# Optimization experiments

Measured on AMD Instinct MI355X. Metric: run time of the kernel, lower is better.

## Reference

```python
import jax, jax.numpy as jnp
import numpy as np

C = 0.1          # curvature
EPS = 1e-8
BN_EPS = 1e-5
MAX_NORM = 0.9

def batchnorm_train(x, gamma, beta):
    mu = jnp.mean(x, axis=0)
    var = jnp.var(x, axis=0)  # biased, matches torch BN normalization
    return gamma * (x - mu) * jax.lax.rsqrt(var + BN_EPS) + beta

def euclidean_to_poincare(x, c=C, max_norm=MAX_NORM):
    norm = jnp.linalg.norm(x, axis=-1, keepdims=True)
    zeros_mask = norm == 0
    safe_norm = jnp.where(zeros_mask, jnp.ones_like(norm), norm)
    sqrt_c = jnp.sqrt(jnp.asarray(c, x.dtype))
    scale = max_norm * jnp.tanh(sqrt_c * norm) / (sqrt_c * safe_norm)
    return jnp.where(zeros_mask, jnp.zeros_like(x), scale * x)

def poincare_to_euclidean(x, c=C):
    norms = jnp.linalg.norm(x, axis=-1, keepdims=True)
    norms = jnp.clip(norms, 1e-8, 1.0 - 1e-8)
    sqrt_c = jnp.sqrt(jnp.asarray(c, x.dtype))
    return x * jnp.arctanh(sqrt_c * norms) / (sqrt_c * norms)

def batch_poincare_exp_map(x, v, c=C):
    x_nsq = jnp.sum(x * x, axis=-1, keepdims=True)
    lambda_x = 2.0 / (1.0 - c * x_nsq + EPS)
    v_norm = jnp.linalg.norm(v, axis=-1, keepdims=True)
    v_norm = jnp.maximum(v_norm, EPS)
    sqrt_c = jnp.sqrt(jnp.asarray(c, x.dtype))
    scale = jnp.tanh(sqrt_c * lambda_x * v_norm / 2.0) / (sqrt_c * v_norm)
    sv = scale * v
    numerator = (1.0 - c * x_nsq) * sv
    x_sv = jnp.sum(x * sv, axis=-1, keepdims=True)
    sv_nsq = jnp.sum(sv * sv, axis=-1, keepdims=True)
    denom = 1.0 - 2.0 * c * x_sv + c * c * x_nsq * sv_nsq
    result = x + numerator / (denom + EPS)
    mask = jnp.all(jnp.isfinite(result), axis=-1, keepdims=True)
    return jnp.where(mask, result, jnp.zeros_like(result))

def batch_poincare_log_map(x, y, c=C):
    x_nsq = jnp.sum(x * x, axis=-1, keepdims=True)
    lambda_x = 2.0 / (1.0 - c * x_nsq + EPS)
    y_nsq = jnp.sum(y * y, axis=-1, keepdims=True)
    xy = jnp.sum(x * y, axis=-1, keepdims=True)
    numerator = (1.0 - 2.0 * c * xy + c * y_nsq) * x - (1.0 - c * x_nsq) * y
    denom = 1.0 - 2.0 * c * xy + c * c * x_nsq * y_nsq
    diff = numerator / (denom + EPS)
    diff_norm = jnp.linalg.norm(diff, axis=-1, keepdims=True)
    diff_norm = jnp.maximum(diff_norm, EPS)
    sqrt_c = jnp.sqrt(jnp.asarray(c, x.dtype))
    return 2.0 / (sqrt_c * lambda_x) * jnp.arctanh(sqrt_c * diff_norm) * diff / diff_norm

def setup_inputs() -> dict:
    key = jax.random.key(0)
    ks = jax.random.split(key, 8)
    B, D_IN, H, D_OUT = 8192, 1024, 2048, 1000
    x = jax.random.normal(ks[0], (B, D_IN), dtype=jnp.float32)
    # kaiming_normal fan_out: std = sqrt(2/fan_out) with fan_out = out_features
    W1 = jax.random.normal(ks[1], (H, D_IN), dtype=jnp.float32) * np.sqrt(2.0 / H)
    b1 = jnp.zeros((H,), jnp.float32)
    g1 = jnp.ones((H,), jnp.float32)
    be1 = jnp.zeros((H,), jnp.float32)
    W2 = jax.random.normal(ks[2], (H, H), dtype=jnp.float32) * np.sqrt(2.0 / H)
    b2 = jnp.zeros((H,), jnp.float32)
    g2 = jnp.ones((H,), jnp.float32)
    be2 = jnp.zeros((H,), jnp.float32)
    W3 = jax.random.normal(ks[3], (D_OUT, H), dtype=jnp.float32) * np.sqrt(2.0 / D_OUT)
    b3 = jnp.zeros((D_OUT,), jnp.float32)
    return {"x": x, "W1": W1, "b1": b1, "g1": g1, "be1": be1,
            "W2": W2, "b2": b2, "g2": g2, "be2": be2, "W3": W3, "b3": b3}

def reference(x, W1, b1, g1, be1, W2, b2, g2, be2, W3, b3):
    h1 = jax.nn.relu(batchnorm_train(x @ W1.T + b1, g1, be1))
    h1_hyp = euclidean_to_poincare(h1)
    origin = jnp.zeros_like(h1_hyp)
    h1_tan = batch_poincare_log_map(origin, h1_hyp)
    h2_tan = jax.nn.relu(batchnorm_train(h1_tan @ W2.T + b2, g2, be2))
    h2_hyp = batch_poincare_exp_map(origin, h2_tan)
    h2_euc = poincare_to_euclidean(h2_hyp)
    out = h2_euc @ W3.T + b3
    return jax.nn.log_softmax(out, axis=1)
```

## Files before the change

kernel.cpp:

```cpp
#include <hip/hip_runtime.h>

typedef __bf16 bf16x8 __attribute__((ext_vector_type(8)));
typedef float f32x16 __attribute__((ext_vector_type(16)));
typedef unsigned short us8 __attribute__((ext_vector_type(8)));

#define AS1 __attribute__((address_space(1)))
#define AS3 __attribute__((address_space(3)))

__device__ __forceinline__ unsigned short f2bf(float x) {
  unsigned int u = __float_as_uint(x);
  u += 0x7fffu + ((u >> 16) & 1u);
  return (unsigned short)(u >> 16);
}
__device__ __forceinline__ float bf2f(unsigned short u) {
  return __uint_as_float(((unsigned int)u) << 16);
}
__device__ __forceinline__ void async_copy16(const void* g, void* l) {
  __builtin_amdgcn_global_load_lds((AS1 void*)(g), (AS3 void*)(l), 16, 0, 0);
}

__global__ void __launch_bounds__(256) k_prep(const float* __restrict__ x,
                                              const float* __restrict__ W1,
                                              const float* __restrict__ W2,
                                              const float* __restrict__ W3,
                                              unsigned short* __restrict__ Xb,
                                              unsigned short* __restrict__ W1b,
                                              unsigned short* __restrict__ W2b,
                                              unsigned short* __restrict__ W3b,
                                              float* __restrict__ P) {
  const long n1 = 2097152, n2 = 524288, n3 = 1048576, n4 = 524288;
  long i = (long)blockIdx.x * 256 + threadIdx.x;
  const float* s = nullptr;
  unsigned short* d = nullptr;
  long j = i;
  if (i < n1)                { s = x;  d = Xb; }
  else if ((j -= n1) < n2)   { s = W1; d = W1b; }
  else if ((j -= n2) < n3)   { s = W2; d = W2b; }
  else if ((j -= n3) < n4) {
    ushort4 o;
    if ((j >> 9) < 1000) {
      float4 v = ((const float4*)W3)[j];
      o.x = f2bf(v.x); o.y = f2bf(v.y); o.z = f2bf(v.z); o.w = f2bf(v.w);
    } else { o.x = 0; o.y = 0; o.z = 0; o.w = 0; }
    ((ushort4*)W3b)[j] = o;
    return;
  } else {
    j -= n4;
    ((float4*)P)[j] = (float4){0.f, 0.f, 0.f, 0.f};
    return;
  }
  float4 v = ((const float4*)s)[j];
  ushort4 o;
  o.x = f2bf(v.x); o.y = f2bf(v.y); o.z = f2bf(v.z); o.w = f2bf(v.w);
  ((ushort4*)d)[j] = o;
}

template <bool OUTBF16, bool STATS>
__global__ void __launch_bounds__(256) k_gemm(const unsigned short* __restrict__ A,
                                              const unsigned short* __restrict__ B,
                                              void* __restrict__ Cout, int K,
                                              int lda, int ldb, int ldc, int nmax,
                                              const float* __restrict__ bias,
                                              float* __restrict__ P) {
  __shared__ __align__(16) unsigned short lA[128 * 64];
  __shared__ __align__(16) unsigned short lB[128 * 64];
  const int tid = threadIdx.x;
  const int wave = tid >> 6;
  const int lane = tid & 63;
  const long m0 = (long)blockIdx.y * 128;
  const long n0 = (long)blockIdx.x * 128;

  const int rsub = lane >> 3;
  const int qg = ((lane & 7) ^ rsub) * 8;
  const unsigned short* gA = A + (m0 + wave * 32 + rsub) * (long)lda + qg;
  const unsigned short* gB = B + (n0 + wave * 32 + rsub) * (long)ldb + qg;
  unsigned short* lAw = lA + (wave * 32) * 64;
  unsigned short* lBw = lB + (wave * 32) * 64;

  const int wr = (wave >> 1) * 64;
  const int wc = (wave & 1) * 64;
  const int l31 = lane & 31;
  const int khalf = lane >> 5;
  const int r7 = l31 & 7;

  f32x16 acc[2][2];
#pragma unroll
  for (int i = 0; i < 2; ++i)
#pragma unroll
    for (int j = 0; j < 2; ++j) acc[i][j] = (f32x16)(0.f);

  for (int k0 = 0; k0 < K; k0 += 64) {
#pragma unroll
    for (int r = 0; r < 4; ++r) {
      async_copy16(gA + (long)(r * 8) * lda + k0, lAw + r * 8 * 64);
      async_copy16(gB + (long)(r * 8) * ldb + k0, lBw + r * 8 * 64);
    }
    __syncthreads();

#pragma unroll
    for (int ks = 0; ks < 4; ++ks) {
      const int off = ((ks * 2 + khalf) ^ r7) * 8;
      bf16x8 af[2], bfr[2];
#pragma unroll
      for (int i = 0; i < 2; ++i)
        af[i] = *(const bf16x8*)&lA[(wr + i * 32 + l31) * 64 + off];
#pragma unroll
      for (int j = 0; j < 2; ++j)
        bfr[j] = *(const bf16x8*)&lB[(wc + j * 32 + l31) * 64 + off];
#pragma unroll
      for (int i = 0; i < 2; ++i)
#pragma unroll
        for (int j = 0; j < 2; ++j)
          acc[i][j] = __builtin_amdgcn_mfma_f32_32x32x16_bf16(af[i], bfr[j], acc[i][j], 0, 0, 0);
    }
    __syncthreads();
  }

  const int rbase = 4 * khalf;
  if (OUTBF16) {
    unsigned short* C = (unsigned short*)Cout;
#pragma unroll
    for (int i = 0; i < 2; ++i)
#pragma unroll
      for (int j = 0; j < 2; ++j) {
        long col = n0 + wc + j * 32 + l31;
#pragma unroll
        for (int reg = 0; reg < 16; ++reg) {
          long row = m0 + wr + i * 32 + (reg & 3) + 8 * (reg >> 2) + rbase;
          C[row * (long)ldc + col] = f2bf(acc[i][j][reg]);
        }
      }
  } else {
    float* C = (float*)Cout;
#pragma unroll
    for (int i = 0; i < 2; ++i)
#pragma unroll
      for (int j = 0; j < 2; ++j) {
        long col = n0 + wc + j * 32 + l31;
        if (col < nmax) {
          float bv = bias ? bias[col] : 0.f;
#pragma unroll
          for (int reg = 0; reg < 16; ++reg) {
            long row = m0 + wr + i * 32 + (reg & 3) + 8 * (reg >> 2) + rbase;
            C[row * (long)ldc + col] = acc[i][j][reg] + bv;
          }
        }
      }
  }

  if (STATS) {
    float* sred = (float*)lA;
    sred[tid] = 0.f;
    __syncthreads();
#pragma unroll
    for (int j = 0; j < 2; ++j) {
      float s = 0.f, s2 = 0.f;
#pragma unroll
      for (int i = 0; i < 2; ++i)
#pragma unroll
        for (int reg = 0; reg < 16; ++reg) {
          float v = acc[i][j][reg];
          s += v;
          s2 = fmaf(v, v, s2);
        }
      int cl = wc + j * 32 + l31;
      atomicAdd(&sred[cl], s);
      atomicAdd(&sred[128 + cl], s2);
    }
    __syncthreads();
    if (tid < 128) {
      atomicAdd(&P[n0 + tid], sred[tid]);
      atomicAdd(&P[2048 + n0 + tid], sred[128 + tid]);
    }
  }
}

__global__ void __launch_bounds__(256) k_bnfin(const float* __restrict__ P,
                                               const float* __restrict__ g,
                                               const float* __restrict__ be,
                                               float* __restrict__ sc,
                                               float* __restrict__ sh) {
  int col = blockIdx.x * 256 + threadIdx.x;
  float mean = P[col] * (1.f / 8192.f);
  float var = P[2048 + col] * (1.f / 8192.f) - mean * mean;
  float rinv = rsqrtf(var + 1e-5f);
  float a = g[col] * rinv;
  sc[col] = a;
  sh[col] = be[col] - mean * a;
}

template <bool STAGE2>
__global__ void __launch_bounds__(256) k_fuse(const unsigned short* __restrict__ Zb,
                                              const float* __restrict__ sc,
                                              const float* __restrict__ sh,
                                              unsigned short* __restrict__ Ab) {
  __shared__ float red[4];
  int row = blockIdx.x, t = threadIdx.x;
  us8 z8 = ((const us8*)(Zb + (long)row * 2048))[t];
  float4 a0 = ((const float4*)sc)[2 * t], a1 = ((const float4*)sc)[2 * t + 1];
  float4 b0 = ((const float4*)sh)[2 * t], b1 = ((const float4*)sh)[2 * t + 1];
  float v[8];
  v[0] = fmaxf(fmaf(bf2f(z8[0]), a0.x, b0.x), 0.f);
  v[1] = fmaxf(fmaf(bf2f(z8[1]), a0.y, b0.y), 0.f);
  v[2] = fmaxf(fmaf(bf2f(z8[2]), a0.z, b0.z), 0.f);
  v[3] = fmaxf(fmaf(bf2f(z8[3]), a0.w, b0.w), 0.f);
  v[4] = fmaxf(fmaf(bf2f(z8[4]), a1.x, b1.x), 0.f);
  v[5] = fmaxf(fmaf(bf2f(z8[5]), a1.y, b1.y), 0.f);
  v[6] = fmaxf(fmaf(bf2f(z8[6]), a1.z, b1.z), 0.f);
  v[7] = fmaxf(fmaf(bf2f(z8[7]), a1.w, b1.w), 0.f);
  float ss = 0.f;
#pragma unroll
  for (int i = 0; i < 8; ++i) ss = fmaf(v[i], v[i], ss);
#pragma unroll
  for (int o = 32; o > 0; o >>= 1) ss += __shfl_down(ss, o, 64);
  if ((t & 63) == 0) red[t >> 6] = ss;
  __syncthreads();
  float n2 = red[0] + red[1] + red[2] + red[3];

  const float rsc = 0.31622776601683794f;
  float fac;
  if (STAGE2) {
    float nn = sqrtf(n2);
    float vn = fmaxf(nn, 1e-8f);
    float tt = rsc * vn;
    float scl = tanhf(tt) / tt;
    float hn = scl * nn;
    float cn = fminf(fmaxf(hn, 1e-8f), 1.0f);
    float z = rsc * cn;
    fac = scl * (atanhf(z) / z);
  } else {
    fac = 0.f;
    if (n2 > 0.f) {
      float n = sqrtf(n2);
      float th = tanhf(rsc * n);
      float s = 0.9f * th / (rsc * n);
      float dn = fmaxf(s * n, 1e-8f);
      float z = rsc * dn;
      fac = -(atanhf(z) / z) * s;
    }
  }
  us8 o8;
#pragma unroll
  for (int i = 0; i < 8; ++i) o8[i] = f2bf(v[i] * fac);
  ((us8*)(Ab + (long)row * 2048))[t] = o8;
}

__global__ void __launch_bounds__(256) k_lsm(const float* __restrict__ Za,
                                             const float* __restrict__ Zb2,
                                             const float* __restrict__ b3,
                                             float* __restrict__ out) {
  __shared__ float red[4];
  int row = blockIdx.x, t = threadIdx.x;
  const float* za = Za + (long)row * 1024;
  const float* zb = Zb2 + (long)row * 1024;
  float v[4];
  float mx = -3.4e38f;
#pragma unroll
  for (int i = 0; i < 4; ++i) {
    int c = t + i * 256;
    v[i] = (c < 1000) ? (za[c] + zb[c] + b3[c]) : -3.4e38f;
    mx = fmaxf(mx, v[i]);
  }
#pragma unroll
  for (int o = 32; o > 0; o >>= 1) mx = fmaxf(mx, __shfl_down(mx, o, 64));
  if ((t & 63) == 0) red[t >> 6] = mx;
  __syncthreads();
  mx = fmaxf(fmaxf(red[0], red[1]), fmaxf(red[2], red[3]));
  __syncthreads();

  float se = 0.f;
#pragma unroll
  for (int i = 0; i < 4; ++i) {
    int c = t + i * 256;
    if (c < 1000) se += expf(v[i] - mx);
  }
#pragma unroll
  for (int o = 32; o > 0; o >>= 1) se += __shfl_down(se, o, 64);
  if ((t & 63) == 0) red[t >> 6] = se;
  __syncthreads();
  float s = red[0] + red[1] + red[2] + red[3];
  float ls = logf(s);
#pragma unroll
  for (int i = 0; i < 4; ++i) {
    int c = t + i * 256;
    if (c < 1000) out[(long)row * 1000 + c] = v[i] - mx - ls;
  }
}

extern "C" void kernel_launch(void* const* d_in, const int* in_sizes, int n_in,
                              void* d_out, int out_size, void* d_ws, size_t ws_size,
                              hipStream_t stream) {
  (void)in_sizes; (void)n_in; (void)out_size; (void)ws_size;
  const float* x   = (const float*)d_in[0];
  const float* W1  = (const float*)d_in[1];
  const float* g1  = (const float*)d_in[3];
  const float* be1 = (const float*)d_in[4];
  const float* W2  = (const float*)d_in[5];
  const float* g2  = (const float*)d_in[7];
  const float* be2 = (const float*)d_in[8];
  const float* W3  = (const float*)d_in[9];
  const float* b3  = (const float*)d_in[10];
  float* out = (float*)d_out;

  char* ws = (char*)d_ws;
  size_t off = 0;
  auto alloc = [&](size_t bytes) {
    void* p = ws + off;
    off += (bytes + 255) & ~(size_t)255;
    return p;
  };
  unsigned short* Xb  = (unsigned short*)alloc((size_t)8192 * 1024 * 2);
  unsigned short* W1b = (unsigned short*)alloc((size_t)2048 * 1024 * 2);
  unsigned short* W2b = (unsigned short*)alloc((size_t)2048 * 2048 * 2);
  unsigned short* W3b = (unsigned short*)alloc((size_t)1024 * 2048 * 2);
  unsigned short* Zb  = (unsigned short*)alloc((size_t)8192 * 2048 * 2);
  unsigned short* Ab  = (unsigned short*)alloc((size_t)8192 * 2048 * 2);
  float* Z3a          = (float*)alloc((size_t)8192 * 1024 * 4);
  float* P            = (float*)alloc((size_t)2 * 4096 * 4);
  float* SC           = (float*)alloc(2048 * 4);
  float* SH           = (float*)alloc(2048 * 4);
  float* P2 = P + 4096;
  float* Z3b = (float*)Zb;

  k_prep<<<16392, 256, 0, stream>>>(x, W1, W2, W3, Xb, W1b, W2b, W3b, P);

  k_gemm<true, true><<<dim3(16, 64), 256, 0, stream>>>(Xb, W1b, Zb, 1024, 1024, 1024, 2048, 2048, nullptr, P);
  k_bnfin<<<8, 256, 0, stream>>>(P, g1, be1, SC, SH);
  k_fuse<false><<<8192, 256, 0, stream>>>(Zb, SC, SH, Ab);

  k_gemm<true, true><<<dim3(16, 64), 256, 0, stream>>>(Ab, W2b, Zb, 2048, 2048, 2048, 2048, 2048, nullptr, P2);
  k_bnfin<<<8, 256, 0, stream>>>(P2, g2, be2, SC, SH);
  k_fuse<true><<<8192, 256, 0, stream>>>(Zb, SC, SH, Ab);

  k_gemm<false, false><<<dim3(8, 64), 256, 0, stream>>>(Ab, W3b, Z3a, 1024, 2048, 2048, 1024, 1024, nullptr, nullptr);
  k_gemm<false, false><<<dim3(8, 64), 256, 0, stream>>>(Ab + 1024, W3b + 1024, Z3b, 1024, 2048, 2048, 1024, 1024, nullptr, nullptr);
  k_lsm<<<8192, 256, 0, stream>>>(Z3a, Z3b, b3, out);
}
```

Before: 361.0 us.

## Fuse BN finalize into row kernels, remap GEMM blocks per XCD, merge split-K launches

Drops the separate BN-finalize kernel. Each fuse block now recomputes the per-column scale and shift from the accumulated stats and processes four rows, one per wave, using wave-level shuffle reductions with no shared memory or barriers. The GEMM remaps block indices so that consecutive M-tiles land on the same XCD for better L2 reuse. The two split-K output GEMMs become one launch using blockIdx.z, and log-softmax likewise moves to one row per wave. The cost is redundant BN-stat recomputation in every fuse block and more registers per thread.

```diff
diff --git a/kernel.cpp b/kernel.cpp
--- a/kernel.cpp
+++ b/kernel.cpp
@@ -58,22 +58,29 @@
 template <bool OUTBF16, bool STATS>
 __global__ void __launch_bounds__(256) k_gemm(const unsigned short* __restrict__ A,
                                               const unsigned short* __restrict__ B,
-                                              void* __restrict__ Cout, int K,
-                                              int lda, int ldb, int ldc, int nmax,
-                                              const float* __restrict__ bias,
+                                              void* __restrict__ Cout,
+                                              void* __restrict__ Cout2, int K,
+                                              int lda, int ldb, int ldc,
                                               float* __restrict__ P) {
   __shared__ __align__(16) unsigned short lA[128 * 64];
   __shared__ __align__(16) unsigned short lB[128 * 64];
   const int tid = threadIdx.x;
   const int wave = tid >> 6;
   const int lane = tid & 63;
-  const long m0 = (long)blockIdx.y * 128;
-  const long n0 = (long)blockIdx.x * 128;
+
+  const int f = blockIdx.x + gridDim.x * blockIdx.y;
+  const int xcd = f & 7;
+  const int fi = f >> 3;
+  const int nblk = fi % gridDim.x;
+  const int mblk = fi / gridDim.x + (gridDim.y >> 3) * xcd;
+  const long m0 = (long)mblk * 128;
+  const long n0 = (long)nblk * 128;
+  const long koff = (long)blockIdx.z * K;
 
   const int rsub = lane >> 3;
   const int qg = ((lane & 7) ^ rsub) * 8;
-  const unsigned short* gA = A + (m0 + wave * 32 + rsub) * (long)lda + qg;
-  const unsigned short* gB = B + (n0 + wave * 32 + rsub) * (long)ldb + qg;
+  const unsigned short* gA = A + (m0 + wave * 32 + rsub) * (long)lda + koff + qg;
+  const unsigned short* gB = B + (n0 + wave * 32 + rsub) * (long)ldb + koff + qg;
   unsigned short* lAw = lA + (wave * 32) * 64;
   unsigned short* lBw = lB + (wave * 32) * 64;
 
@@ -131,19 +138,16 @@
         }
       }
   } else {
-    float* C = (float*)Cout;
+    float* C = (float*)(blockIdx.z ? Cout2 : Cout);
 #pragma unroll
     for (int i = 0; i < 2; ++i)
 #pragma unroll
       for (int j = 0; j < 2; ++j) {
         long col = n0 + wc + j * 32 + l31;
-        if (col < nmax) {
-          float bv = bias ? bias[col] : 0.f;
-#pragma unroll
-          for (int reg = 0; reg < 16; ++reg) {
-            long row = m0 + wr + i * 32 + (reg & 3) + 8 * (reg >> 2) + rbase;
-            C[row * (long)ldc + col] = acc[i][j][reg] + bv;
-          }
+#pragma unroll
+        for (int reg = 0; reg < 16; ++reg) {
+          long row = m0 + wr + i * 32 + (reg & 3) + 8 * (reg >> 2) + rbase;
+          C[row * (long)ldc + col] = acc[i][j][reg];
         }
       }
   }
@@ -175,47 +179,53 @@
   }
 }
 
-__global__ void __launch_bounds__(256) k_bnfin(const float* __restrict__ P,
-                                               const float* __restrict__ g,
-                                               const float* __restrict__ be,
-                                               float* __restrict__ sc,
-                                               float* __restrict__ sh) {
-  int col = blockIdx.x * 256 + threadIdx.x;
-  float mean = P[col] * (1.f / 8192.f);
-  float var = P[2048 + col] * (1.f / 8192.f) - mean * mean;
-  float rinv = rsqrtf(var + 1e-5f);
-  float a = g[col] * rinv;
-  sc[col] = a;
-  sh[col] = be[col] - mean * a;
-}
-
 template <bool STAGE2>
 __global__ void __launch_bounds__(256) k_fuse(const unsigned short* __restrict__ Zb,
-                                              const float* __restrict__ sc,
-                                              const float* __restrict__ sh,
+                                              const float* __restrict__ P,
+                                              const float* __restrict__ g,
+                                              const float* __restrict__ be,
                                               unsigned short* __restrict__ Ab) {
-  __shared__ float red[4];
-  int row = blockIdx.x, t = threadIdx.x;
-  us8 z8 = ((const us8*)(Zb + (long)row * 2048))[t];
-  float4 a0 = ((const float4*)sc)[2 * t], a1 = ((const float4*)sc)[2 * t + 1];
-  float4 b0 = ((const float4*)sh)[2 * t], b1 = ((const float4*)sh)[2 * t + 1];
-  float v[8];
-  v[0] = fmaxf(fmaf(bf2f(z8[0]), a0.x, b0.x), 0.f);
-  v[1] = fmaxf(fmaf(bf2f(z8[1]), a0.y, b0.y), 0.f);
-  v[2] = fmaxf(fmaf(bf2f(z8[2]), a0.z, b0.z), 0.f);
-  v[3] = fmaxf(fmaf(bf2f(z8[3]), a0.w, b0.w), 0.f);
-  v[4] = fmaxf(fmaf(bf2f(z8[4]), a1.x, b1.x), 0.f);
-  v[5] = fmaxf(fmaf(bf2f(z8[5]), a1.y, b1.y), 0.f);
-  v[6] = fmaxf(fmaf(bf2f(z8[6]), a1.z, b1.z), 0.f);
-  v[7] = fmaxf(fmaf(bf2f(z8[7]), a1.w, b1.w), 0.f);
+  const int t = threadIdx.x, wave = t >> 6, lane = t & 63;
+  const long row = (long)blockIdx.x * 4 + wave;
+
+  float sc[32], sh[32];
+#pragma unroll
+  for (int c = 0; c < 4; ++c) {
+    int b4 = (lane + 64 * c) * 2;
+    float4 s0 = ((const float4*)P)[b4],       s1 = ((const float4*)P)[b4 + 1];
+    float4 q0 = ((const float4*)P)[512 + b4], q1 = ((const float4*)P)[512 + b4 + 1];
+    float4 g0 = ((const float4*)g)[b4],       g1 = ((const float4*)g)[b4 + 1];
+    float4 e0 = ((const float4*)be)[b4],      e1 = ((const float4*)be)[b4 + 1];
+    float sm[8] = {s0.x, s0.y, s0.z, s0.w, s1.x, s1.y, s1.z, s1.w};
+    float sq[8] = {q0.x, q0.y, q0.z, q0.w, q1.x, q1.y, q1.z, q1.w};
+    float gg[8] = {g0.x, g0.y, g0.z, g0.w, g1.x, g1.y, g1.z, g1.w};
+    float bb[8] = {e0.x, e0.y, e0.z, e0.w, e1.x, e1.y, e1.z, e1.w};
+#pragma unroll
+    for (int j = 0; j < 8; ++j) {
+      float mean = sm[j] * (1.f / 8192.f);
+      float var = sq[j] * (1.f / 8192.f) - mean * mean;
+      float a = gg[j] * rsqrtf(var + 1e-5f);
+      sc[c * 8 + j] = a;
+      sh[c * 8 + j] = bb[j] - mean * a;
+    }
+  }
+
+  const us8* zr = (const us8*)(Zb + row * 2048);
+  float v[32];
   float ss = 0.f;
 #pragma unroll
-  for (int i = 0; i < 8; ++i) ss = fmaf(v[i], v[i], ss);
-#pragma unroll
-  for (int o = 32; o > 0; o >>= 1) ss += __shfl_down(ss, o, 64);
-  if ((t & 63) == 0) red[t >> 6] = ss;
-  __syncthreads();
-  float n2 = red[0] + red[1] + red[2] + red[3];
+  for (int c = 0; c < 4; ++c) {
+    us8 z8 = zr[lane + 64 * c];
+#pragma unroll
+    for (int j = 0; j < 8; ++j) {
+      float xv = fmaxf(fmaf(bf2f(z8[j]), sc[c * 8 + j], sh[c * 8 + j]), 0.f);
+      v[c * 8 + j] = xv;
+      ss = fmaf(xv, xv, ss);
+    }
+  }
+#pragma unroll
+  for (int o = 32; o > 0; o >>= 1) ss += __shfl_xor(ss, o, 64);
+  float n2 = ss;
 
   const float rsc = 0.31622776601683794f;
   float fac;
@@ -239,51 +249,52 @@
       fac = -(atanhf(z) / z) * s;
     }
   }
-  us8 o8;
-#pragma unroll
-  for (int i = 0; i < 8; ++i) o8[i] = f2bf(v[i] * fac);
-  ((us8*)(Ab + (long)row * 2048))[t] = o8;
+  us8* dr = (us8*)(Ab + row * 2048);
+#pragma unroll
+  for (int c = 0; c < 4; ++c) {
+    us8 o8;
+#pragma unroll
+    for (int j = 0; j < 8; ++j) o8[j] = f2bf(v[c * 8 + j] * fac);
+    dr[lane + 64 * c] = o8;
+  }
 }
 
 __global__ void __launch_bounds__(256) k_lsm(const float* __restrict__ Za,
                                              const float* __restrict__ Zb2,
                                              const float* __restrict__ b3,
                                              float* __restrict__ out) {
-  __shared__ float red[4];
-  int row = blockIdx.x, t = threadIdx.x;
-  const float* za = Za + (long)row * 1024;
-  const float* zb = Zb2 + (long)row * 1024;
-  float v[4];
+  const int t = threadIdx.x, wave = t >> 6, lane = t & 63;
+  const long row = (long)blockIdx.x * 4 + wave;
+  const float* za = Za + row * 1024;
+  const float* zb = Zb2 + row * 1024;
+  float v[16];
   float mx = -3.4e38f;
 #pragma unroll
-  for (int i = 0; i < 4; ++i) {
-    int c = t + i * 256;
-    v[i] = (c < 1000) ? (za[c] + zb[c] + b3[c]) : -3.4e38f;
-    mx = fmaxf(mx, v[i]);
-  }
-#pragma unroll
-  for (int o = 32; o > 0; o >>= 1) mx = fmaxf(mx, __shfl_down(mx, o, 64));
-  if ((t & 63) == 0) red[t >> 6] = mx;
-  __syncthreads();
-  mx = fmaxf(fmaxf(red[0], red[1]), fmaxf(red[2], red[3]));
-  __syncthreads();
+  for (int c = 0; c < 16; ++c) {
+    int col = lane + 64 * c;
+    if (col < 1000) {
+      v[c] = za[col] + zb[col] + b3[col];
+      mx = fmaxf(mx, v[c]);
+    } else v[c] = -3.4e38f;
+  }
+#pragma unroll
+  for (int o = 32; o > 0; o >>= 1) mx = fmaxf(mx, __shfl_xor(mx, o, 64));
 
   float se = 0.f;
 #pragma unroll
-  for (int i = 0; i < 4; ++i) {
-    int c = t + i * 256;
-    if (c < 1000) se += expf(v[i] - mx);
-  }
-#pragma unroll
-  for (int o = 32; o > 0; o >>= 1) se += __shfl_down(se, o, 64);
-  if ((t & 63) == 0) red[t >> 6] = se;
-  __syncthreads();
-  float s = red[0] + red[1] + red[2] + red[3];
-  float ls = logf(s);
-#pragma unroll
-  for (int i = 0; i < 4; ++i) {
-    int c = t + i * 256;
-    if (c < 1000) out[(long)row * 1000 + c] = v[i] - mx - ls;
+  for (int c = 0; c < 16; ++c) {
+    int col = lane + 64 * c;
+    if (col < 1000) se += expf(v[c] - mx);
+  }
+#pragma unroll
+  for (int o = 32; o > 0; o >>= 1) se += __shfl_xor(se, o, 64);
+  float ls = logf(se);
+
+  float* orow = out + row * 1000;
+#pragma unroll
+  for (int c = 0; c < 16; ++c) {
+    int col = lane + 64 * c;
+    if (col < 1000) orow[col] = v[c] - mx - ls;
   }
 }
 
@@ -317,22 +328,17 @@
   unsigned short* Ab  = (unsigned short*)alloc((size_t)8192 * 2048 * 2);
   float* Z3a          = (float*)alloc((size_t)8192 * 1024 * 4);
   float* P            = (float*)alloc((size_t)2 * 4096 * 4);
-  float* SC           = (float*)alloc(2048 * 4);
-  float* SH           = (float*)alloc(2048 * 4);
   float* P2 = P + 4096;
   float* Z3b = (float*)Zb;
 
   k_prep<<<16392, 256, 0, stream>>>(x, W1, W2, W3, Xb, W1b, W2b, W3b, P);
 
-  k_gemm<true, true><<<dim3(16, 64), 256, 0, stream>>>(Xb, W1b, Zb, 1024, 1024, 1024, 2048, 2048, nullptr, P);
-  k_bnfin<<<8, 256, 0, stream>>>(P, g1, be1, SC, SH);
-  k_fuse<false><<<8192, 256, 0, stream>>>(Zb, SC, SH, Ab);
-
-  k_gemm<true, true><<<dim3(16, 64), 256, 0, stream>>>(Ab, W2b, Zb, 2048, 2048, 2048, 2048, 2048, nullptr, P2);
-  k_bnfin<<<8, 256, 0, stream>>>(P2, g2, be2, SC, SH);
-  k_fuse<true><<<8192, 256, 0, stream>>>(Zb, SC, SH, Ab);
-
-  k_gemm<false, false><<<dim3(8, 64), 256, 0, stream>>>(Ab, W3b, Z3a, 1024, 2048, 2048, 1024, 1024, nullptr, nullptr);
-  k_gemm<false, false><<<dim3(8, 64), 256, 0, stream>>>(Ab + 1024, W3b + 1024, Z3b, 1024, 2048, 2048, 1024, 1024, nullptr, nullptr);
-  k_lsm<<<8192, 256, 0, stream>>>(Z3a, Z3b, b3, out);
-}
+  k_gemm<true, true><<<dim3(16, 64, 1), 256, 0, stream>>>(Xb, W1b, Zb, Zb, 1024, 1024, 1024, 2048, P);
+  k_fuse<false><<<2048, 256, 0, stream>>>(Zb, P, g1, be1, Ab);
+
+  k_gemm<true, true><<<dim3(16, 64, 1), 256, 0, stream>>>(Ab, W2b, Zb, Zb, 2048, 2048, 2048, 2048, P2);
+  k_fuse<true><<<2048, 256, 0, stream>>>(Zb, P2, g2, be2, Ab);
+
+  k_gemm<false, false><<<dim3(8, 64, 2), 256, 0, stream>>>(Ab, W3b, Z3a, Z3b, 1024, 2048, 2048, 1024, nullptr);
+  k_lsm<<<2048, 256, 0, stream>>>(Z3a, Z3b, b3, out);
+}
```

New measurement: 355.8 us. Within noise of the previous version (-1.5%).
